# Performance work log

Measured on AMD Instinct MI355X. Metric: run time of the kernel, lower is better.

## Reference

```python
import jax, jax.numpy as jnp
import numpy as np

N_NODES = 50000
NEG_SLOPE = 0.2


def gat_conv(x, src, dst, W, al, ar, b):
    """DGL-style GATConv. x:[N,Fin] W:[Fin,H*D] al,ar:[H,D] b:[H*D] -> [N,H,D]."""
    H, D = al.shape
    feat = (x @ W).reshape(-1, H, D)                      # [N,H,D]
    el = jnp.sum(feat * al, axis=-1)                      # [N,H]
    er = jnp.sum(feat * ar, axis=-1)                      # [N,H]
    e = jax.nn.leaky_relu(el[src] + er[dst], NEG_SLOPE)   # [E,H] per-edge scores
    # segment softmax over incoming edges of each dst node
    m = jax.ops.segment_max(e, dst, num_segments=N_NODES)  # [N,H] (-inf for empty)
    ex = jnp.exp(e - m[dst])                              # [E,H]
    s = jax.ops.segment_sum(ex, dst, num_segments=N_NODES)  # [N,H]
    alpha = ex / s[dst]                                   # [E,H]
    msg = alpha[:, :, None] * feat[src]                   # [E,H,D]
    out = jax.ops.segment_sum(msg, dst, num_segments=N_NODES)  # [N,H,D]
    return out + b.reshape(1, H, D)


def setup_inputs() -> dict:
    key = jax.random.key(0)
    ks = jax.random.split(key, 12)
    E = 800000
    inp = {
        "x": jax.random.normal(ks[0], (N_NODES, 128), jnp.float32),
        "W1": jax.random.normal(ks[1], (2, 128, 128), jnp.float32) * 0.1,
        "al1": jax.random.normal(ks[2], (2, 4, 32), jnp.float32) * 0.1,
        "ar1": jax.random.normal(ks[3], (2, 4, 32), jnp.float32) * 0.1,
        "b1": jnp.zeros((2, 128), jnp.float32),
        "W2": jax.random.normal(ks[4], (2, 128, 64), jnp.float32) * 0.1,
        "al2": jax.random.normal(ks[5], (2, 1, 64), jnp.float32) * 0.1,
        "ar2": jax.random.normal(ks[6], (2, 1, 64), jnp.float32) * 0.1,
        "b2": jnp.zeros((2, 64), jnp.float32),
        "src": jax.random.randint(ks[7], (2, E), 0, N_NODES, jnp.int32),
        "dst": jax.random.randint(ks[8], (2, E), 0, N_NODES, jnp.int32),
    }
    return inp


def reference(x, W1, al1, ar1, b1, W2, al2, ar2, b2, src, dst):
    R = src.shape[0]  # number of meta-path relations
    # layer 1: HeteroGraphConv(sum over relations) -> elu(flatten heads)
    h1 = sum(gat_conv(x, src[r], dst[r], W1[r], al1[r], ar1[r], b1[r])
             for r in range(R))                           # [N,4,32]
    h1 = jax.nn.elu(h1.reshape(N_NODES, -1))              # [N,128]
    # layer 2: single head, mean over head dim
    h2 = sum(gat_conv(h1, src[r], dst[r], W2[r], al2[r], ar2[r], b2[r])
             for r in range(R))                           # [N,1,64]
    return jnp.mean(h2, axis=1)                           # [N,64]
```

## Files before the change

### kernel.cpp

```cpp
#include <hip/hip_runtime.h>
#include <hip/hip_bf16.h>
#include <math.h>

using bf16x8 = __attribute__((ext_vector_type(8))) short;
using f32x4  = __attribute__((ext_vector_type(4))) float;
using v4i    = __attribute__((ext_vector_type(4))) int;

#define NCH 32
#define SCAN_B 1024

__device__ __forceinline__ float b2f(unsigned short u) {
    return __uint_as_float(((unsigned)u) << 16);
}
__device__ __forceinline__ unsigned short f2b(float f) {
    unsigned u = __float_as_uint(f);
    return (unsigned short)((u + 0x7fff + ((u >> 16) & 1)) >> 16);
}

__global__ void k_prep(const float* __restrict__ x, unsigned short* __restrict__ xb, int n8,
                       const float* __restrict__ W1, const float* __restrict__ W2,
                       unsigned short* __restrict__ wt1, unsigned short* __restrict__ wt2,
                       unsigned* __restrict__ cnt, int ncnt, int nbx, int nbw) {
    int bid = blockIdx.x;
    if (bid < nbx) {
        int i = bid * 256 + threadIdx.x;
        if (i >= n8) return;
        float4 a = ((const float4*)x)[i * 2], b = ((const float4*)x)[i * 2 + 1];
        uint4 o;
        o.x = f2b(a.x) | ((unsigned)f2b(a.y) << 16);
        o.y = f2b(a.z) | ((unsigned)f2b(a.w) << 16);
        o.z = f2b(b.x) | ((unsigned)f2b(b.y) << 16);
        o.w = f2b(b.z) | ((unsigned)f2b(b.w) << 16);
        ((uint4*)xb)[i] = o;
    } else if (bid < nbx + nbw) {
        int i = (bid - nbx) * 256 + threadIdx.x;
        if (i < 32768) {
            int r = i >> 14, c = (i >> 7) & 127, k = i & 127;
            wt1[i] = f2b(W1[(r << 14) + (k << 7) + c]);
        } else {
            int j = i - 32768;
            if (j >= 16384) return;
            int r = j >> 13, c = (j >> 7) & 63, k = j & 127;
            wt2[j] = f2b(W2[r * 8192 + k * 64 + c]);
        }
    } else {
        int i = (bid - nbx - nbw) * 256 + threadIdx.x;
        if (i < ncnt) cnt[i] = 0u;
    }
}

__global__ __launch_bounds__(256) void k_histp(const int* __restrict__ dst,
                                               unsigned* __restrict__ cnt, int E, int N) {
    __shared__ unsigned sm[6250];
    const int part = blockIdx.x & 7, chunk = blockIdx.x >> 3;
    const int r = blockIdx.y;
    const int P = N / 8;
    const int lo = part * P;
    for (int i = threadIdx.x; i < P; i += 256) sm[i] = 0u;
    __syncthreads();
    const int per = E / 32;
    const int e0 = chunk * per, e1 = e0 + per;
    const int* dr = dst + (size_t)r * E;
    for (int e = e0 + (int)threadIdx.x * 4; e < e1; e += 1024) {
        v4i d4 = *(const v4i*)(dr + e);
        int a0 = d4.x - lo, a1 = d4.y - lo, a2 = d4.z - lo, a3 = d4.w - lo;
        if ((unsigned)a0 < (unsigned)P) atomicAdd(&sm[a0], 1u);
        if ((unsigned)a1 < (unsigned)P) atomicAdd(&sm[a1], 1u);
        if ((unsigned)a2 < (unsigned)P) atomicAdd(&sm[a2], 1u);
        if ((unsigned)a3 < (unsigned)P) atomicAdd(&sm[a3], 1u);
    }
    __syncthreads();
    unsigned* cr = cnt + (size_t)r * N + lo;
    for (int i = threadIdx.x; i < P; i += 256) {
        unsigned v = sm[i];
        if (v) atomicAdd(&cr[i], v);
    }
}

__global__ void k_scanA(const unsigned* __restrict__ cnt, unsigned* __restrict__ bsum,
                        int n, int nb) {
    int r = blockIdx.y, b = blockIdx.x;
    int i0 = b * SCAN_B;
    unsigned s = 0;
    for (int t = threadIdx.x; t < SCAN_B; t += 256) {
        int i = i0 + t;
        if (i < n) s += cnt[(size_t)r * n + i];
    }
    __shared__ unsigned red[256];
    red[threadIdx.x] = s; __syncthreads();
    for (int st = 128; st > 0; st >>= 1) {
        if ((int)threadIdx.x < st) red[threadIdx.x] += red[threadIdx.x + st];
        __syncthreads();
    }
    if (threadIdx.x == 0) bsum[r * nb + b] = red[0];
}

__global__ void k_scanC2(unsigned* __restrict__ cnt, const unsigned* __restrict__ bsum,
                         unsigned* __restrict__ off, int n, int nb) {
    int r = blockIdx.y, b = blockIdx.x;
    __shared__ unsigned sbase[65];
    if (threadIdx.x < 64) {
        int l = threadIdx.x;
        unsigned orig = (l < nb) ? bsum[r * nb + l] : 0u;
        unsigned v = orig;
        for (int st = 1; st < 64; st <<= 1) {
            unsigned t = __shfl_up(v, st);
            if (l >= st) v += t;
        }
        sbase[l] = v - orig;
        if (l == 63) sbase[64] = v;
    }
    __syncthreads();
    if (b == 0 && threadIdx.x == 0) off[(size_t)r * (n + 1) + n] = sbase[64];
    const unsigned base = sbase[b];
    int i0 = b * SCAN_B + (int)threadIdx.x * 4;
    unsigned v[4]; unsigned s = 0;
#pragma unroll
    for (int j = 0; j < 4; j++) {
        int i = i0 + j;
        v[j] = (i < n) ? cnt[(size_t)r * n + i] : 0u;
        s += v[j];
    }
    __shared__ unsigned red[256];
    red[threadIdx.x] = s; __syncthreads();
    for (int st = 1; st < 256; st <<= 1) {
        unsigned t = ((int)threadIdx.x >= st) ? red[threadIdx.x - st] : 0u;
        __syncthreads();
        red[threadIdx.x] += t;
        __syncthreads();
    }
    unsigned run = base + red[threadIdx.x] - s;
#pragma unroll
    for (int j = 0; j < 4; j++) {
        int i = i0 + j;
        if (i < n) {
            off[(size_t)r * (n + 1) + i] = run;
            cnt[(size_t)r * n + i] = run;
        }
        run += v[j];
    }
}

__device__ __forceinline__ void scat_body(int bid, const int* __restrict__ src,
                                          const int* __restrict__ dst, unsigned* __restrict__ cur,
                                          unsigned short* __restrict__ csr, int E, int N) {
    const int part = bid & 7;
    const int q = bid >> 3;
    const int r = q & 1, chunk = q >> 1;
    const int lo = part * (N / 8), hi = lo + N / 8;
    const int per = E / NCH;
    const int e0 = chunk * per, e1 = e0 + per;
    const int* dr = dst + (size_t)r * E;
    const int* sr = src + (size_t)r * E;
    unsigned* curr = cur + (size_t)r * N;
    unsigned short* csrr = csr + (size_t)r * E;
    for (int e = e0 + (int)threadIdx.x * 4; e < e1; e += 1024) {
        v4i d4 = *(const v4i*)(dr + e);
        bool m0 = (d4.x >= lo) & (d4.x < hi);
        bool m1 = (d4.y >= lo) & (d4.y < hi);
        bool m2 = (d4.z >= lo) & (d4.z < hi);
        bool m3 = (d4.w >= lo) & (d4.w < hi);
        if (m0 | m1 | m2 | m3) {
            v4i s4 = *(const v4i*)(sr + e);
            if (m0) { unsigned p = atomicAdd(&curr[d4.x], 1u);
                      __builtin_nontemporal_store((unsigned short)s4.x, &csrr[p]); }
            if (m1) { unsigned p = atomicAdd(&curr[d4.y], 1u);
                      __builtin_nontemporal_store((unsigned short)s4.y, &csrr[p]); }
            if (m2) { unsigned p = atomicAdd(&curr[d4.z], 1u);
                      __builtin_nontemporal_store((unsigned short)s4.z, &csrr[p]); }
            if (m3) { unsigned p = atomicAdd(&curr[d4.w], 1u);
                      __builtin_nontemporal_store((unsigned short)s4.w, &csrr[p]); }
        }
    }
}

template <int M, int H>
__device__ __forceinline__ void gemm_body(int xblk, int r,
        const unsigned short* __restrict__ Xb, const unsigned short* __restrict__ Wt0,
        const float* __restrict__ alv, const float* __restrict__ arv,
        unsigned short* __restrict__ feat0, float* __restrict__ el, float* __restrict__ er,
        int N, unsigned short* xs, unsigned short* ws) {
    constexpr int D = M / H;
    const unsigned short* Wt = Wt0 + (size_t)r * M * 128;
    unsigned short* outp = feat0 + (size_t)r * N * M;
    float* elr = el + (size_t)r * N * H;
    float* err = er + (size_t)r * N * H;
    const int tid = threadIdx.x;
    const int row0 = xblk * 64;
    for (int ch = tid; ch < 64 * 16; ch += 256) {
        int rr = ch >> 4, c16 = ch & 15;
        int gr = row0 + rr;
        uint4 v = make_uint4(0, 0, 0, 0);
        if (gr < N) v = ((const uint4*)(Xb + (size_t)gr * 128))[c16];
        int byte = rr * 256 + ((c16 * 16) ^ ((rr & 7) << 4));
        *(uint4*)((char*)xs + byte) = v;
    }
    for (int ch = tid; ch < M * 16; ch += 256) {
        int rr = ch >> 4, c16 = ch & 15;
        uint4 v = ((const uint4*)(Wt + (size_t)rr * 128))[c16];
        int byte = rr * 256 + ((c16 * 16) ^ ((rr & 7) << 4));
        *(uint4*)((char*)ws + byte) = v;
    }
    __syncthreads();
    const int w = tid >> 6, l = tid & 63;
    const int sub = l & 15;
    const int ar_ = w * 16 + sub;
    const int kg = l >> 4;
    bf16x8 a[4];
#pragma unroll
    for (int k4 = 0; k4 < 4; k4++) {
        int byte = ar_ * 256 + (((kg * 16) + k4 * 64) ^ ((ar_ & 7) << 4));
        a[k4] = *(const bf16x8*)((const char*)xs + byte);
    }
    float alr[M / 16], arr[M / 16];
#pragma unroll
    for (int ct = 0; ct < M / 16; ct++) {
        alr[ct] = alv[(size_t)r * M + ct * 16 + sub];
        arr[ct] = arv[(size_t)r * M + ct * 16 + sub];
    }
    float pel[H][4], per[H][4];
#pragma unroll
    for (int h = 0; h < H; h++)
#pragma unroll
        for (int q = 0; q < 4; q++) { pel[h][q] = 0.f; per[h][q] = 0.f; }

#pragma unroll
    for (int ct = 0; ct < M / 16; ct++) {
        f32x4 acc = {0.f, 0.f, 0.f, 0.f};
        const int bc = ct * 16 + sub;
#pragma unroll
        for (int k4 = 0; k4 < 4; k4++) {
            int byte = bc * 256 + (((kg * 16) + k4 * 64) ^ ((bc & 7) << 4));
            bf16x8 bfr = *(const bf16x8*)((const char*)ws + byte);
            acc = __builtin_amdgcn_mfma_f32_16x16x32_bf16(a[k4], bfr, acc, 0, 0, 0);
        }
        const int hct = (ct * 16) / D;
#pragma unroll
        for (int q = 0; q < 4; q++) {
            pel[hct][q] += acc[q] * alr[ct];
            per[hct][q] += acc[q] * arr[ct];
        }
#pragma unroll
        for (int q = 0; q < 4; q++) {
            int gr = row0 + w * 16 + kg * 4 + q;
            if (gr < N) outp[(size_t)gr * M + ct * 16 + sub] = f2b(acc[q]);
        }
    }
#pragma unroll
    for (int h = 0; h < H; h++)
#pragma unroll
        for (int q = 0; q < 4; q++) {
            float v = pel[h][q], u = per[h][q];
#pragma unroll
            for (int o = 8; o > 0; o >>= 1) { v += __shfl_xor(v, o); u += __shfl_xor(u, o); }
            pel[h][q] = v; per[h][q] = u;
        }
#pragma unroll
    for (int h = 0; h < H; h++) {
        if (sub == h) {
#pragma unroll
            for (int q = 0; q < 4; q++) {
                int gr = row0 + w * 16 + kg * 4 + q;
                if (gr < N) { elr[(size_t)gr * H + h] = pel[h][q]; err[(size_t)gr * H + h] = per[h][q]; }
            }
        }
    }
}

__global__ __launch_bounds__(256) void k_scatgemm(
    const int* __restrict__ src, const int* __restrict__ dst,
    unsigned* __restrict__ cur, unsigned short* __restrict__ csr, int E, int N, int scatBlocks,
    const unsigned short* __restrict__ Xb, const unsigned short* __restrict__ Wt0,
    const float* __restrict__ alv, const float* __restrict__ arv,
    unsigned short* __restrict__ feat0, float* __restrict__ el, float* __restrict__ er) {
    __shared__ __align__(16) unsigned short xs[64 * 128];
    __shared__ __align__(16) unsigned short ws[128 * 128];
    int bid = blockIdx.x;
    if (bid < scatBlocks) {
        scat_body(bid, src, dst, cur, csr, E, N);
    } else {
        int g = bid - scatBlocks;
        gemm_body<128, 4>(g >> 1, g & 1, Xb, Wt0, alv, arv, feat0, el, er, N, xs, ws);
    }
}

__global__ __launch_bounds__(256) void k_gemm2(
    const unsigned short* __restrict__ Xb, const unsigned short* __restrict__ Wt0,
    const float* __restrict__ alv, const float* __restrict__ arv,
    unsigned short* __restrict__ feat0, float* __restrict__ el, float* __restrict__ er, int N) {
    __shared__ __align__(16) unsigned short xs[64 * 128];
    __shared__ __align__(16) unsigned short ws[64 * 128];
    gemm_body<64, 1>(blockIdx.x, blockIdx.y, Xb, Wt0, alv, arv, feat0, el, er, N, xs, ws);
}

template <int ELUF>
__global__ __launch_bounds__(256) void k_node_gat1(
    const unsigned* __restrict__ off, const unsigned short* __restrict__ csr_src,
    const float* __restrict__ el, const float* __restrict__ er,
    const unsigned short* __restrict__ feat0, const unsigned short* __restrict__ feat1,
    const float* __restrict__ bias, unsigned* __restrict__ outp, int N, int E) {
    constexpr int H = 4, HD = 128;
    __shared__ float s_w[4][4 * 64];
    __shared__ int s_sid[4][64];
    const int wslot = threadIdx.x >> 6;
    const int lane = threadIdx.x & 63;
    const int n = (blockIdx.x * 256 + threadIdx.x) >> 6;
    if (n >= N) return;
    const int c0 = lane * 2;
    const int h = c0 / 32;
    const unsigned laneoff = (unsigned)lane << 2;

    float res[2] = {0.f, 0.f};

    for (int r = 0; r < 2; r++) {
        const char* __restrict__ featc = (const char*)(r ? feat1 : feat0);
        const float* elr = el + (size_t)r * N * H;
        const float* ernp = er + (size_t)r * N * H + (size_t)n * H;
        float ern[H];
#pragma unroll
        for (int hh = 0; hh < H; hh++) ern[hh] = ernp[hh];
        const unsigned* offr = off + (size_t)r * (N + 1);
        const unsigned short* srcs = csr_src + (size_t)r * E;
        const unsigned o0 = offr[n], o1 = offr[n + 1];

        float den = 0.f;
        float acc[2] = {0.f, 0.f};

        for (unsigned base = o0; base < o1; base += 64) {
            const int cnt = (int)min(64u, o1 - base);
            if (lane < cnt) {
                unsigned sv = srcs[base + lane];
                s_sid[wslot][lane] = (int)sv;
                float4 e4 = *(const float4*)(elr + (size_t)sv * 4);
                float v0 = e4.x + ern[0]; v0 = v0 > 0.f ? v0 : 0.2f * v0;
                float v1 = e4.y + ern[1]; v1 = v1 > 0.f ? v1 : 0.2f * v1;
                float v2 = e4.z + ern[2]; v2 = v2 > 0.f ? v2 : 0.2f * v2;
                float v3 = e4.w + ern[3]; v3 = v3 > 0.f ? v3 : 0.2f * v3;
                float4 wv = make_float4(__expf(v0), __expf(v1), __expf(v2), __expf(v3));
                *(float4*)&s_w[wslot][lane * 4] = wv;
            }
            asm volatile("s_waitcnt lgkmcnt(0)" ::: "memory");
#pragma unroll 8
            for (int j = 0; j < cnt; j++) {
                unsigned sv = (unsigned)s_sid[wslot][j];
                float wv = s_w[wslot][j * 4 + h];
                den += wv;
                unsigned u = *(const unsigned*)(featc + ((sv << 8) + laneoff));
                acc[0] += wv * __uint_as_float(u << 16);
                acc[1] += wv * __uint_as_float(u & 0xffff0000u);
            }
        }
        if (den > 0.f) {
            float inv = 1.f / den;
            res[0] += acc[0] * inv;
            res[1] += acc[1] * inv;
        }
    }
    float v0 = res[0] + bias[c0] + bias[HD + c0];
    float v1 = res[1] + bias[c0 + 1] + bias[HD + c0 + 1];
    if (ELUF) { v0 = v0 > 0.f ? v0 : expm1f(v0); v1 = v1 > 0.f ? v1 : expm1f(v1); }
    outp[((size_t)n * HD + c0) / 2] = f2b(v0) | ((unsigned)f2b(v1) << 16);
}

__global__ __launch_bounds__(256) void k_node_gat2(
    const unsigned* __restrict__ off, const unsigned short* __restrict__ csr_src,
    const float* __restrict__ el, const float* __restrict__ er,
    const unsigned short* __restrict__ feat0, const unsigned short* __restrict__ feat1,
    const float* __restrict__ bias, float* __restrict__ outp, int N, int E) {
    __shared__ uint2 s_ws[4][64];
    const int wslot = threadIdx.x >> 6;
    const int lane = threadIdx.x & 63;
    const int n = (blockIdx.x * 256 + threadIdx.x) >> 6;
    if (n >= N) return;
    const int sub = lane & 15, quarter = lane >> 4;
    const unsigned laneoff = (unsigned)sub << 3;

    float res[4] = {0.f, 0.f, 0.f, 0.f};

    for (int r = 0; r < 2; r++) {
        const char* __restrict__ featc = (const char*)(r ? feat1 : feat0);
        const float* elr = el + (size_t)r * N;
        const float ern = er[(size_t)r * N + n];
        const unsigned* offr = off + (size_t)r * (N + 1);
        const unsigned short* srcs = csr_src + (size_t)r * E;
        const unsigned o0 = offr[n], o1 = offr[n + 1];

        float den = 0.f;
        float acc[4] = {0.f, 0.f, 0.f, 0.f};

        for (unsigned base = o0; base < o1; base += 64) {
            const int cnt = (int)min(64u, o1 - base);
            if (lane < cnt) {
                unsigned sv = srcs[base + lane];
                float v = elr[sv] + ern; v = v > 0.f ? v : 0.2f * v;
                s_ws[wslot][lane] = make_uint2(sv, __float_as_uint(__expf(v)));
            }
            asm volatile("s_waitcnt lgkmcnt(0)" ::: "memory");
#pragma unroll 4
            for (int j4 = 0; j4 < cnt; j4 += 4) {
                int jj = j4 + quarter;
                int jjc = jj < cnt ? jj : 0;
                uint2 sw = s_ws[wslot][jjc];
                float wv = (jj < cnt) ? __uint_as_float(sw.y) : 0.f;
                den += wv;
                uint2 u = *(const uint2*)(featc + (((size_t)sw.x << 7) + laneoff));
                acc[0] += wv * __uint_as_float(u.x << 16);
                acc[1] += wv * __uint_as_float(u.x & 0xffff0000u);
                acc[2] += wv * __uint_as_float(u.y << 16);
                acc[3] += wv * __uint_as_float(u.y & 0xffff0000u);
            }
        }
#pragma unroll
        for (int f = 0; f < 4; f++) {
            acc[f] += __shfl_xor(acc[f], 16);
            acc[f] += __shfl_xor(acc[f], 32);
        }
        den += __shfl_xor(den, 16);
        den += __shfl_xor(den, 32);
        if (den > 0.f) {
            float inv = 1.f / den;
#pragma unroll
            for (int f = 0; f < 4; f++) res[f] += acc[f] * inv;
        }
    }
    if (quarter == 0) {
        int c = sub * 4;
        float4 o;
        o.x = res[0] + bias[c] + bias[64 + c];
        o.y = res[1] + bias[c + 1] + bias[64 + c + 1];
        o.z = res[2] + bias[c + 2] + bias[64 + c + 2];
        o.w = res[3] + bias[c + 3] + bias[64 + c + 3];
        *(float4*)(outp + (size_t)n * 64 + c) = o;
    }
}

extern "C" void kernel_launch(void* const* d_in, const int* in_sizes, int n_in,
                              void* d_out, int out_size, void* d_ws, size_t ws_size,
                              hipStream_t stream) {
    const float* x   = (const float*)d_in[0];
    const float* W1  = (const float*)d_in[1];
    const float* al1 = (const float*)d_in[2];
    const float* ar1 = (const float*)d_in[3];
    const float* b1  = (const float*)d_in[4];
    const float* W2  = (const float*)d_in[5];
    const float* al2 = (const float*)d_in[6];
    const float* ar2 = (const float*)d_in[7];
    const float* b2  = (const float*)d_in[8];
    const int* src   = (const int*)d_in[9];
    const int* dst   = (const int*)d_in[10];

    const int N = in_sizes[0] / 128;
    const int E = in_sizes[9] / 2;
    float* out = (float*)d_out;

    char* w = (char*)d_ws;
    unsigned short* xb   = (unsigned short*)w; w += (size_t)N * 128 * 2;
    unsigned short* feat = (unsigned short*)w; w += (size_t)2 * N * 128 * 2;
    unsigned short* h1b  = (unsigned short*)w; w += (size_t)N * 128 * 2;
    unsigned short* wt1  = (unsigned short*)w; w += (size_t)2 * 128 * 128 * 2;
    unsigned short* wt2  = (unsigned short*)w; w += (size_t)2 * 64 * 128 * 2;
    float* el      = (float*)w; w += (size_t)2 * N * 4 * 4;
    float* er      = (float*)w; w += (size_t)2 * N * 4 * 4;
    unsigned* cnt  = (unsigned*)w; w += (size_t)2 * N * 4;
    unsigned* off  = (unsigned*)w; w += (size_t)2 * (N + 1) * 4;
    unsigned* bsum = (unsigned*)w; w += 2 * 64 * 4;
    unsigned short* csr_src = (unsigned short*)w; w += (size_t)2 * E * 2;

    auto cdiv = [](long long a, long long b) { return (int)((a + b - 1) / b); };
    const int NB = cdiv(N, SCAN_B);

    const int nbx = cdiv((long long)N * 16, 256);
    const int nbw = cdiv(49152, 256);
    const int nbz = cdiv(2LL * N, 256);
    k_prep<<<nbx + nbw + nbz, 256, 0, stream>>>(x, xb, N * 16, W1, W2, wt1, wt2, cnt, 2 * N, nbx, nbw);

    { dim3 g(32 * 8, 2); k_histp<<<g, 256, 0, stream>>>(dst, cnt, E, N); }
    { dim3 g(NB, 2); k_scanA<<<g, 256, 0, stream>>>(cnt, bsum, N, NB); }
    { dim3 g(NB, 2); k_scanC2<<<g, 256, 0, stream>>>(cnt, bsum, off, N, NB); }

    const int scatBlocks = NCH * 8 * 2;
    const int gemmBlocks = cdiv(N, 64) * 2;
    k_scatgemm<<<scatBlocks + gemmBlocks, 256, 0, stream>>>(
        src, dst, cnt, csr_src, E, N, scatBlocks, xb, wt1, al1, ar1, feat, el, er);

    k_node_gat1<1><<<cdiv(N, 4), 256, 0, stream>>>(off, csr_src, el, er,
        feat, feat + (size_t)N * 128, b1, (unsigned*)h1b, N, E);

    { dim3 g(cdiv(N, 64), 2);
      k_gemm2<<<g, 256, 0, stream>>>(h1b, wt2, al2, ar2, feat, el, er, N); }
    k_node_gat2<<<cdiv(N, 4), 256, 0, stream>>>(off, csr_src, el, er,
        feat, feat + (size_t)N * 64, b2, out, N, E);
}
```

Baseline: 239.8 us.

## Fuse block-sum scan into histogram kernel and share X tile across relations in gemm2

The histogram kernel now uses 4 node partitions with larger shared histograms and also computes per-1024-node block sums, adding them atomically into bsum. This removes the separate scanA kernel launch and its re-read of the counts. bsum is moved so the prep kernel zeroes it together with cnt. gemm2 is rewritten as a single kernel per row tile that loads the h1 tile into registers once and loops over both relations, halving X traffic and blocks at the cost of less parallelism.

```diff
diff --git a/kernel.cpp b/kernel.cpp
--- a/kernel.cpp
+++ b/kernel.cpp
@@ -50,49 +50,51 @@
 }
 
 __global__ __launch_bounds__(256) void k_histp(const int* __restrict__ dst,
-                                               unsigned* __restrict__ cnt, int E, int N) {
-    __shared__ unsigned sm[6250];
-    const int part = blockIdx.x & 7, chunk = blockIdx.x >> 3;
+                                               unsigned* __restrict__ cnt,
+                                               unsigned* __restrict__ bsum,
+                                               int E, int N, int nb) {
+    __shared__ unsigned sm[12500];
+    __shared__ unsigned wsum[4];
+    const int group = blockIdx.x & 3, chunk = blockIdx.x >> 2;
     const int r = blockIdx.y;
-    const int P = N / 8;
-    const int lo = part * P;
-    for (int i = threadIdx.x; i < P; i += 256) sm[i] = 0u;
+    const int P2 = N / 4;
+    const int lo = group * P2;
+    const int tid = threadIdx.x;
+    for (int i = tid; i < P2; i += 256) sm[i] = 0u;
     __syncthreads();
     const int per = E / 32;
     const int e0 = chunk * per, e1 = e0 + per;
     const int* dr = dst + (size_t)r * E;
-    for (int e = e0 + (int)threadIdx.x * 4; e < e1; e += 1024) {
+    for (int e = e0 + tid * 4; e < e1; e += 1024) {
         v4i d4 = *(const v4i*)(dr + e);
         int a0 = d4.x - lo, a1 = d4.y - lo, a2 = d4.z - lo, a3 = d4.w - lo;
-        if ((unsigned)a0 < (unsigned)P) atomicAdd(&sm[a0], 1u);
-        if ((unsigned)a1 < (unsigned)P) atomicAdd(&sm[a1], 1u);
-        if ((unsigned)a2 < (unsigned)P) atomicAdd(&sm[a2], 1u);
-        if ((unsigned)a3 < (unsigned)P) atomicAdd(&sm[a3], 1u);
+        if ((unsigned)a0 < (unsigned)P2) atomicAdd(&sm[a0], 1u);
+        if ((unsigned)a1 < (unsigned)P2) atomicAdd(&sm[a1], 1u);
+        if ((unsigned)a2 < (unsigned)P2) atomicAdd(&sm[a2], 1u);
+        if ((unsigned)a3 < (unsigned)P2) atomicAdd(&sm[a3], 1u);
     }
     __syncthreads();
     unsigned* cr = cnt + (size_t)r * N + lo;
-    for (int i = threadIdx.x; i < P; i += 256) {
+    for (int i = tid; i < P2; i += 256) {
         unsigned v = sm[i];
         if (v) atomicAdd(&cr[i], v);
     }
-}
-
-__global__ void k_scanA(const unsigned* __restrict__ cnt, unsigned* __restrict__ bsum,
-                        int n, int nb) {
-    int r = blockIdx.y, b = blockIdx.x;
-    int i0 = b * SCAN_B;
-    unsigned s = 0;
-    for (int t = threadIdx.x; t < SCAN_B; t += 256) {
-        int i = i0 + t;
-        if (i < n) s += cnt[(size_t)r * n + i];
-    }
-    __shared__ unsigned red[256];
-    red[threadIdx.x] = s; __syncthreads();
-    for (int st = 128; st > 0; st >>= 1) {
-        if ((int)threadIdx.x < st) red[threadIdx.x] += red[threadIdx.x + st];
+    const int rg0 = lo >> 10, rg1 = (lo + P2 - 1) >> 10;
+    for (int rg = rg0; rg <= rg1; rg++) {
+        int i0 = rg * 1024 - lo; if (i0 < 0) i0 = 0;
+        int i1 = (rg + 1) * 1024 - lo; if (i1 > P2) i1 = P2;
+        unsigned s = 0;
+        for (int i = i0 + tid; i < i1; i += 256) s += sm[i];
+#pragma unroll
+        for (int o = 32; o > 0; o >>= 1) s += __shfl_xor(s, o);
+        if ((tid & 63) == 0) wsum[tid >> 6] = s;
         __syncthreads();
-    }
-    if (threadIdx.x == 0) bsum[r * nb + b] = red[0];
+        if (tid == 0) {
+            unsigned t = wsum[0] + wsum[1] + wsum[2] + wsum[3];
+            if (t) atomicAdd(&bsum[r * nb + rg], t);
+        }
+        __syncthreads();
+    }
 }
 
 __global__ void k_scanC2(unsigned* __restrict__ cnt, const unsigned* __restrict__ bsum,
@@ -285,12 +287,86 @@
 }
 
 __global__ __launch_bounds__(256) void k_gemm2(
-    const unsigned short* __restrict__ Xb, const unsigned short* __restrict__ Wt0,
+    const unsigned short* __restrict__ Xb, const unsigned short* __restrict__ wt2,
     const float* __restrict__ alv, const float* __restrict__ arv,
     unsigned short* __restrict__ feat0, float* __restrict__ el, float* __restrict__ er, int N) {
     __shared__ __align__(16) unsigned short xs[64 * 128];
     __shared__ __align__(16) unsigned short ws[64 * 128];
-    gemm_body<64, 1>(blockIdx.x, blockIdx.y, Xb, Wt0, alv, arv, feat0, el, er, N, xs, ws);
+    const int tid = threadIdx.x;
+    const int row0 = blockIdx.x * 64;
+    for (int ch = tid; ch < 64 * 16; ch += 256) {
+        int rr = ch >> 4, c16 = ch & 15;
+        int gr = row0 + rr;
+        uint4 v = make_uint4(0, 0, 0, 0);
+        if (gr < N) v = ((const uint4*)(Xb + (size_t)gr * 128))[c16];
+        int byte = rr * 256 + ((c16 * 16) ^ ((rr & 7) << 4));
+        *(uint4*)((char*)xs + byte) = v;
+    }
+    __syncthreads();
+    const int w = tid >> 6, l = tid & 63;
+    const int sub = l & 15, kg = l >> 4;
+    const int ar_ = w * 16 + sub;
+    bf16x8 a[4];
+#pragma unroll
+    for (int k4 = 0; k4 < 4; k4++) {
+        int byte = ar_ * 256 + (((kg * 16) + k4 * 64) ^ ((ar_ & 7) << 4));
+        a[k4] = *(const bf16x8*)((const char*)xs + byte);
+    }
+    for (int r = 0; r < 2; r++) {
+        for (int ch = tid; ch < 64 * 16; ch += 256) {
+            int rr = ch >> 4, c16 = ch & 15;
+            uint4 v = ((const uint4*)(wt2 + (size_t)r * 8192 + (size_t)rr * 128))[c16];
+            int byte = rr * 256 + ((c16 * 16) ^ ((rr & 7) << 4));
+            *(uint4*)((char*)ws + byte) = v;
+        }
+        __syncthreads();
+        unsigned short* outp = feat0 + (size_t)r * N * 64;
+        float alr[4], arr[4];
+#pragma unroll
+        for (int ct = 0; ct < 4; ct++) {
+            alr[ct] = alv[(size_t)r * 64 + ct * 16 + sub];
+            arr[ct] = arv[(size_t)r * 64 + ct * 16 + sub];
+        }
+        float pel[4] = {0.f, 0.f, 0.f, 0.f}, per[4] = {0.f, 0.f, 0.f, 0.f};
+#pragma unroll
+        for (int ct = 0; ct < 4; ct++) {
+            f32x4 acc = {0.f, 0.f, 0.f, 0.f};
+            const int bc = ct * 16 + sub;
+#pragma unroll
+            for (int k4 = 0; k4 < 4; k4++) {
+                int byte = bc * 256 + (((kg * 16) + k4 * 64) ^ ((bc & 7) << 4));
+                bf16x8 bfr = *(const bf16x8*)((const char*)ws + byte);
+                acc = __builtin_amdgcn_mfma_f32_16x16x32_bf16(a[k4], bfr, acc, 0, 0, 0);
+            }
+#pragma unroll
+            for (int q = 0; q < 4; q++) {
+                pel[q] += acc[q] * alr[ct];
+                per[q] += acc[q] * arr[ct];
+            }
+#pragma unroll
+            for (int q = 0; q < 4; q++) {
+                int gr = row0 + w * 16 + kg * 4 + q;
+                if (gr < N) outp[(size_t)gr * 64 + ct * 16 + sub] = f2b(acc[q]);
+            }
+        }
+#pragma unroll
+        for (int q = 0; q < 4; q++) {
+            float v = pel[q], u = per[q];
+#pragma unroll
+            for (int o = 8; o > 0; o >>= 1) { v += __shfl_xor(v, o); u += __shfl_xor(u, o); }
+            pel[q] = v; per[q] = u;
+        }
+        if (sub == 0) {
+            float* elr = el + (size_t)r * N;
+            float* err = er + (size_t)r * N;
+#pragma unroll
+            for (int q = 0; q < 4; q++) {
+                int gr = row0 + w * 16 + kg * 4 + q;
+                if (gr < N) { elr[gr] = pel[q]; err[gr] = per[q]; }
+            }
+        }
+        __syncthreads();
+    }
 }
 
 template <int ELUF>
@@ -462,20 +538,20 @@
     float* el      = (float*)w; w += (size_t)2 * N * 4 * 4;
     float* er      = (float*)w; w += (size_t)2 * N * 4 * 4;
     unsigned* cnt  = (unsigned*)w; w += (size_t)2 * N * 4;
+    unsigned* bsum = (unsigned*)w; w += 2 * 64 * 4;
     unsigned* off  = (unsigned*)w; w += (size_t)2 * (N + 1) * 4;
-    unsigned* bsum = (unsigned*)w; w += 2 * 64 * 4;
     unsigned short* csr_src = (unsigned short*)w; w += (size_t)2 * E * 2;
 
     auto cdiv = [](long long a, long long b) { return (int)((a + b - 1) / b); };
     const int NB = cdiv(N, SCAN_B);
 
+    const int ncnt = 2 * N + 2 * 64;
     const int nbx = cdiv((long long)N * 16, 256);
     const int nbw = cdiv(49152, 256);
-    const int nbz = cdiv(2LL * N, 256);
-    k_prep<<<nbx + nbw + nbz, 256, 0, stream>>>(x, xb, N * 16, W1, W2, wt1, wt2, cnt, 2 * N, nbx, nbw);
-
-    { dim3 g(32 * 8, 2); k_histp<<<g, 256, 0, stream>>>(dst, cnt, E, N); }
-    { dim3 g(NB, 2); k_scanA<<<g, 256, 0, stream>>>(cnt, bsum, N, NB); }
+    const int nbz = cdiv(ncnt, 256);
+    k_prep<<<nbx + nbw + nbz, 256, 0, stream>>>(x, xb, N * 16, W1, W2, wt1, wt2, cnt, ncnt, nbx, nbw);
+
+    { dim3 g(4 * 32, 2); k_histp<<<g, 256, 0, stream>>>(dst, cnt, bsum, E, N, NB); }
     { dim3 g(NB, 2); k_scanC2<<<g, 256, 0, stream>>>(cnt, bsum, off, N, NB); }
 
     const int scatBlocks = NCH * 8 * 2;
@@ -486,8 +562,7 @@
     k_node_gat1<1><<<cdiv(N, 4), 256, 0, stream>>>(off, csr_src, el, er,
         feat, feat + (size_t)N * 128, b1, (unsigned*)h1b, N, E);
 
-    { dim3 g(cdiv(N, 64), 2);
-      k_gemm2<<<g, 256, 0, stream>>>(h1b, wt2, al2, ar2, feat, el, er, N); }
+    k_gemm2<<<cdiv(N, 64), 256, 0, stream>>>(h1b, wt2, al2, ar2, feat, el, er, N);
     k_node_gat2<<<cdiv(N, 4), 256, 0, stream>>>(off, csr_src, el, er,
         feat, feat + (size_t)N * 64, b2, out, N, E);
 }
```

After: 245.3 us. 2.3% more time.
